# Performance work log

Hardware: AMD Instinct MI355X
Metric: run time of the kernel (lower is better)

Reference implementation:

```python
import jax, jax.numpy as jnp
import numpy as np

N_E = 8192
E_DIM = 64
BETA = 0.25
DIVERSITY_GAMMA = 1.0
INV_TEMP = 100.0
EPS = 1e-05


def _entropy(p):
    # matches torch: (-p * log(clamp(p, min=eps))).sum(-1)
    return (-p * jnp.log(jnp.clip(p, EPS))).sum(axis=-1)


def setup_inputs() -> dict:
    key = jax.random.key(0)
    k1, k2 = jax.random.split(key)
    z = jax.random.normal(k1, (16, E_DIM, 32, 32), dtype=jnp.float32)
    # codebook, init like nn.Embedding then uniform_(-1/n_e, 1/n_e) scale doesn't matter for math;
    # use a small uniform init faithful to the module
    emb = jax.random.uniform(k2, (N_E, E_DIM), dtype=jnp.float32,
                             minval=-1.0 / N_E, maxval=1.0 / N_E)
    return {"z": z, "emb": emb}


def reference(z, emb):
    sg = jax.lax.stop_gradient
    # b c h w -> b h w c
    zp = jnp.transpose(z, (0, 2, 3, 1))            # [B,H,W,C]
    zf = zp.reshape(-1, E_DIM)                      # [N, C]
    # pairwise squared distances: ||z||^2 + ||e||^2 - 2 z e^T
    d = (jnp.sum(zf * zf, axis=1, keepdims=True)
         + jnp.sum(emb * emb, axis=1)
         - 2.0 * jnp.einsum('nd,kd->nk', zf, emb))  # [N, n_e]
    min_indices = jnp.argmin(d, axis=1)             # [N]
    z_q = emb[min_indices].reshape(zp.shape)        # gather, [B,H,W,C]
    # legacy commitment loss
    loss = (jnp.mean((sg(z_q) - zp) ** 2)
            + BETA * jnp.mean((z_q - sg(zp)) ** 2))
    # entropy aux loss (frac_per_sample_entropy == 1.0)
    prob = jax.nn.softmax(-d * INV_TEMP, axis=-1)   # [N, n_e]
    per_sample_entropy = _entropy(prob).mean()
    avg_prob = prob.mean(axis=0)                    # [n_e]
    codebook_entropy = _entropy(avg_prob)
    entropy_aux = per_sample_entropy - DIVERSITY_GAMMA * codebook_entropy
    # straight-through estimator
    z_q = zp + sg(z_q - zp)
    quantized = jnp.transpose(z_q, (0, 3, 1, 2))    # b h w c -> b c h w
    return quantized, loss, entropy_aux, min_indices
```

## Files before the change

kernel.cpp:

```cpp
#include <hip/hip_runtime.h>
#include <cfloat>


typedef __attribute__((ext_vector_type(8))) short short8v;
typedef __attribute__((ext_vector_type(4))) float f32x4;

#define C100L2E 144.26950408889634f
#define C200L2E 288.53900817779268f
#define LN2 0.6931471805599453

#define BLOB_TILE 33792
#define OFF_BLOB   0
#define OFF_INVZ   2162688
#define OFF_MINIDX 2228224
#define OFF_AVG    2293760
#define OFF_PSE    2326528
#define OFF_ZPART  2326544
#define OFF_S1PART (OFF_ZPART + 262144)
#define OFF_DMPART (OFF_S1PART + 262144)
#define OFF_IMPART (OFF_DMPART + 262144)
#define OFF_LOSSP  (OFF_IMPART + 262144)
#define OFF_ZZ     (OFF_LOSSP + 32768)

__device__ __forceinline__ unsigned short f2bf_rne(float f) {
    unsigned u = __float_as_uint(f);
    u = (u + 0x7fffu + ((u >> 16) & 1u)) >> 16;
    return (unsigned short)u;
}

__device__ __forceinline__ void gload_lds16(const void* g, void* l) {
    __builtin_amdgcn_global_load_lds(
        (const __attribute__((address_space(1))) unsigned int*)g,
        (__attribute__((address_space(3))) unsigned int*)l, 16, 0, 0);
}

__global__ __launch_bounds__(256) void k_prep(
    const float* __restrict__ emb, const float* __restrict__ z,
    char* __restrict__ blob, char* __restrict__ zblob, float* __restrict__ zz)
{
    if (blockIdx.x < 32) {
        const int k = blockIdx.x * 256 + threadIdx.x;
        const float* row = emb + k * 64;
        float fv[64];
#pragma unroll
        for (int i = 0; i < 16; ++i) {
            float4 v = ((const float4*)row)[i];
            fv[4 * i] = v.x; fv[4 * i + 1] = v.y; fv[4 * i + 2] = v.z; fv[4 * i + 3] = v.w;
        }
        float r8[8];
#pragma unroll
        for (int j = 0; j < 8; ++j) r8[j] = __fmul_rn(fv[j], fv[j]);
#pragma unroll
        for (int i = 8; i < 64; i += 8)
#pragma unroll
            for (int j = 0; j < 8; ++j)
                r8[j] = __fadd_rn(r8[j], __fmul_rn(fv[i + j], fv[i + j]));
        float s01 = __fadd_rn(r8[0], r8[1]), s23 = __fadd_rn(r8[2], r8[3]);
        float s45 = __fadd_rn(r8[4], r8[5]), s67 = __fadd_rn(r8[6], r8[7]);
        float e2 = __fadd_rn(__fadd_rn(s01, s23), __fadd_rn(s45, s67));

        char* tb = blob + (size_t)(k >> 7) * BLOB_TILE;
        const int r = k & 127;
        ((float*)(tb + 32768))[r] = e2;
        ((float*)(tb + 33280))[r] = e2 * C100L2E;
        const int sw = (r & 7) << 4;
#pragma unroll
        for (int dh = 0; dh < 2; ++dh)
#pragma unroll
            for (int cg = 0; cg < 4; ++cg) {
                short8v hv, lv;
#pragma unroll
                for (int e = 0; e < 8; ++e) {
                    float f = fv[dh * 32 + cg * 8 + e];
                    unsigned short hb = f2bf_rne(f);
                    float hf = __uint_as_float((unsigned)hb << 16);
                    hv[e] = (short)hb;
                    lv[e] = (short)f2bf_rne(f - hf);
                }
                const int byt = (r * 128 + dh * 64 + cg * 16) ^ sw;
                *(short8v*)(tb + byt) = hv;
                *(short8v*)(tb + 16384 + byt) = lv;
            }
    } else {
        const int r = (blockIdx.x - 32) * 256 + threadIdx.x;
        const float* src = z + (r >> 10) * 65536 + (r & 1023);
        float fv[64];
#pragma unroll
        for (int c = 0; c < 64; ++c) fv[c] = src[c * 1024];

        float r8[8];
#pragma unroll
        for (int j = 0; j < 8; ++j) r8[j] = __fmul_rn(fv[j], fv[j]);
#pragma unroll
        for (int i = 8; i < 64; i += 8)
#pragma unroll
            for (int j = 0; j < 8; ++j)
                r8[j] = __fadd_rn(r8[j], __fmul_rn(fv[i + j], fv[i + j]));
        float s01 = __fadd_rn(r8[0], r8[1]), s23 = __fadd_rn(r8[2], r8[3]);
        float s45 = __fadd_rn(r8[4], r8[5]), s67 = __fadd_rn(r8[6], r8[7]);
        zz[r] = __fadd_rn(__fadd_rn(s01, s23), __fadd_rn(s45, s67));

        char* tb = zblob + (size_t)(r >> 6) * 16384;
        const int rowp = r & 63;
#pragma unroll
        for (int cg = 0; cg < 8; ++cg) {
            short8v hv, lv;
#pragma unroll
            for (int e = 0; e < 8; ++e) {
                float f = fv[cg * 8 + e];
                unsigned short hb = f2bf_rne(f);
                float hf = __uint_as_float((unsigned)hb << 16);
                hv[e] = (short)hb;
                lv[e] = (short)f2bf_rne(f - hf);
            }
            *(short8v*)(tb + rowp * 128 + cg * 16) = hv;
            *(short8v*)(tb + 8192 + rowp * 128 + cg * 16) = lv;
        }
    }
}

#define STAGE_EMB(DSTBASE, TILE)                                                  \
    {                                                                             \
        const char* gsrc = blob + (size_t)(TILE) * BLOB_TILE;                     \
        char* ldst = (DSTBASE) + ((tid >> 6) << 10);                              \
        const char* g = gsrc + tid * 16;                                          \
        _Pragma("unroll")                                                         \
        for (int q = 0; q < 8; ++q)                                               \
            gload_lds16(g + q * 4096, ldst + q * 4096);                           \
        if (tid < 64) gload_lds16(gsrc + 32768 + (tid & 63) * 16,                 \
                                  (DSTBASE) + 32768);                             \
    }

#define STAGE512(DSTBASE, TILE)                                                   \
    {                                                                             \
        const char* gsrc = blob + (size_t)(TILE) * BLOB_TILE;                     \
        char* ldst = (DSTBASE) + ((tid >> 6) << 12);                              \
        const char* g = gsrc + ((tid >> 6) << 12) + (tid & 63) * 16;              \
        _Pragma("unroll")                                                         \
        for (int q = 0; q < 4; ++q)                                               \
            gload_lds16(g + q * 1024, ldst + q * 1024);                           \
        if (tid < 64) gload_lds16(gsrc + 32768 + (tid & 63) * 16,                 \
                                  (DSTBASE) + 32768);                             \
    }

__global__ __launch_bounds__(512) void k_pass1(
    const char* __restrict__ zblob, const char* __restrict__ blob,
    const float* __restrict__ zz,
    float* __restrict__ Zpart, float* __restrict__ S1part,
    float* __restrict__ dmpart, int* __restrict__ impart)
{
    __shared__ __align__(16) char smem[2 * BLOB_TILE];

    const int tid = threadIdx.x;
    const int panel = blockIdx.x >> 2;
    const int ks = blockIdx.x & 3;
    const int n0 = panel * 128;

    const int ln = tid & 63, wv = tid >> 6;
    const int lr = ln & 15, lg = ln >> 4;

    short8v Ah[2], Al[2];
    {
        const int p64 = (n0 >> 6) + (wv >> 2);
        const int rowp = (wv & 3) * 16 + lr;
        const char* tb = zblob + (size_t)p64 * 16384;
#pragma unroll
        for (int s = 0; s < 2; ++s) {
            const int byt = rowp * 128 + s * 64 + lg * 16;
            Ah[s] = *(const short8v*)(tb + byt);
            Al[s] = *(const short8v*)(tb + 8192 + byt);
        }
    }
    float zzr[4];
#pragma unroll
    for (int rg = 0; rg < 4; ++rg)
        zzr[rg] = zz[n0 + wv * 16 + lg * 4 + rg];

    STAGE512(smem, ks * 16);

    float Zp[4] = {0.f, 0.f, 0.f, 0.f}, S1p[4] = {0.f, 0.f, 0.f, 0.f};
    float dmin[4] = {FLT_MAX, FLT_MAX, FLT_MAX, FLT_MAX};
    int imin[4] = {0, 0, 0, 0};

    for (int it = 0; it < 16; ++it) {
        const int kbase = ks * 2048 + it * 128;
        __syncthreads();
        const char* bb = smem + (it & 1) * BLOB_TILE;
        if (it < 15) STAGE512(smem + ((it + 1) & 1) * BLOB_TILE, ks * 16 + it + 1);

        f32x4 acc[8];
#pragma unroll
        for (int f = 0; f < 8; ++f) { f32x4 zv = {0.f, 0.f, 0.f, 0.f}; acc[f] = zv; }

#pragma unroll
        for (int f = 0; f < 8; ++f) {
            const int rr = f * 16 + lr;
            const int sw2 = (rr & 7) << 4;
            short8v Bh[2], Bl[2];
#pragma unroll
            for (int s = 0; s < 2; ++s) {
                const int byt = (rr * 128 + s * 64 + lg * 16) ^ sw2;
                Bh[s] = *(const short8v*)(bb + byt);
                Bl[s] = *(const short8v*)(bb + 16384 + byt);
            }
#pragma unroll
            for (int s = 0; s < 2; ++s) {
                acc[f] = __builtin_amdgcn_mfma_f32_16x16x32_bf16(Ah[s], Bh[s], acc[f], 0, 0, 0);
                acc[f] = __builtin_amdgcn_mfma_f32_16x16x32_bf16(Ah[s], Bl[s], acc[f], 0, 0, 0);
                acc[f] = __builtin_amdgcn_mfma_f32_16x16x32_bf16(Al[s], Bh[s], acc[f], 0, 0, 0);
                acc[f] = __builtin_amdgcn_mfma_f32_16x16x32_bf16(Al[s], Bl[s], acc[f], 0, 0, 0);
            }
        }

#pragma unroll
        for (int f = 0; f < 8; ++f) {
            const float e2v = *(const float*)(bb + 32768 + (f * 16 + lr) * 4);
            const float c2 = *(const float*)(bb + 33280 + (f * 16 + lr) * 4);
            const int kk = kbase + f * 16 + lr;
#pragma unroll
            for (int rg = 0; rg < 4; ++rg) {
                const float sdot = acc[f][rg];
                const float t = fmaf(sdot, C200L2E, -c2);
                const float ex = __builtin_amdgcn_exp2f(t);
                Zp[rg] += ex;
                S1p[rg] = fmaf(t, ex, S1p[rg]);
                const float pre = __fadd_rn(zzr[rg], e2v);
                const float dnp = fmaf(-2.f, sdot, pre);
                if (dnp < dmin[rg]) { dmin[rg] = dnp; imin[rg] = kk; }
            }
        }
    }

#pragma unroll
    for (int msk = 1; msk < 16; msk <<= 1) {
#pragma unroll
        for (int rg = 0; rg < 4; ++rg) {
            float d2 = __shfl_xor(dmin[rg], msk, 16);
            int i2 = __shfl_xor(imin[rg], msk, 16);
            float Z2 = __shfl_xor(Zp[rg], msk, 16);
            float s2 = __shfl_xor(S1p[rg], msk, 16);
            if (d2 < dmin[rg] || (d2 == dmin[rg] && i2 < imin[rg])) {
                dmin[rg] = d2; imin[rg] = i2;
            }
            Zp[rg] += Z2;
            S1p[rg] += s2;
        }
    }
    if (lr == 0) {
#pragma unroll
        for (int rg = 0; rg < 4; ++rg) {
            const int n = n0 + wv * 16 + lg * 4 + rg;
            Zpart[ks * 16384 + n] = Zp[rg];
            S1part[ks * 16384 + n] = S1p[rg];
            dmpart[ks * 16384 + n] = dmin[rg];
            impart[ks * 16384 + n] = imin[rg];
        }
    }
}

__global__ __launch_bounds__(256) void k_rowred(
    const float* __restrict__ Zpart, const float* __restrict__ S1part,
    const float* __restrict__ dmpart, const int* __restrict__ impart,
    float* __restrict__ invZ, int* __restrict__ minidx,
    float* __restrict__ out_idx, double* __restrict__ pse_sum)
{
    const int n = blockIdx.x * 256 + threadIdx.x;
    float Z = __fadd_rn(__fadd_rn(Zpart[n], Zpart[16384 + n]),
                        __fadd_rn(Zpart[32768 + n], Zpart[49152 + n]));
    float S1 = __fadd_rn(__fadd_rn(S1part[n], S1part[16384 + n]),
                         __fadd_rn(S1part[32768 + n], S1part[49152 + n]));
    float dm = dmpart[n];
    int im = impart[n];
#pragma unroll
    for (int ksp = 1; ksp < 4; ++ksp) {
        float d2 = dmpart[ksp * 16384 + n];
        int i2 = impart[ksp * 16384 + n];
        if (d2 < dm || (d2 == dm && i2 < im)) { dm = d2; im = i2; }
    }
    minidx[n] = im;
    out_idx[n] = (float)im;
    float iz = 1.0f / Z;
    invZ[n] = iz;
    double h = log((double)Z) - LN2 * (double)S1 * (double)iz;
#pragma unroll
    for (int m = 32; m > 0; m >>= 1) h += __shfl_xor(h, m, 64);
    if ((threadIdx.x & 63) == 0) atomicAdd(pse_sum, h);
}

__global__ __launch_bounds__(256) void k_pass2(
    const char* __restrict__ zblob, const char* __restrict__ blob,
    const float* __restrict__ invZ, float* __restrict__ avg_acc)
{
    __shared__ __align__(16) char smem[BLOB_TILE + 4096];
    float* izAll = (float*)(smem + BLOB_TILE);

    const int tid = threadIdx.x;
    const int kt = blockIdx.x & 63;
    const int ns = blockIdx.x >> 6;
    const int ln = tid & 63, wv = tid >> 6;
    const int lr = ln & 15, lg = ln >> 4;

    STAGE_EMB(smem, kt);
    gload_lds16((const char*)(invZ + ns * 1024) + tid * 16,
                (char*)izAll + (wv << 10));
    __syncthreads();

    float c2v[8];
#pragma unroll
    for (int f = 0; f < 8; ++f)
        c2v[f] = *(const float*)(smem + 33280 + (f * 16 + lr) * 4);

    float acck[8] = {0.f, 0.f, 0.f, 0.f, 0.f, 0.f, 0.f, 0.f};

#pragma unroll 1
    for (int it = 0; it < 16; ++it) {
        const char* tb = zblob + (size_t)(ns * 16 + it) * 16384;
        const int rowp = wv * 16 + lr;
        short8v Ah[2], Al[2];
#pragma unroll
        for (int s = 0; s < 2; ++s) {
            const int byt = rowp * 128 + s * 64 + lg * 16;
            Ah[s] = *(const short8v*)(tb + byt);
            Al[s] = *(const short8v*)(tb + 8192 + byt);
        }
        float4 iz = *(const float4*)&izAll[it * 64 + wv * 16 + lg * 4];
        float izr[4] = {iz.x, iz.y, iz.z, iz.w};

        f32x4 acc[8];
#pragma unroll
        for (int f = 0; f < 8; ++f) { f32x4 zv = {0.f, 0.f, 0.f, 0.f}; acc[f] = zv; }

#pragma unroll
        for (int f = 0; f < 8; ++f) {
            const int rr = f * 16 + lr;
            const int sw2 = (rr & 7) << 4;
            short8v Bh[2], Bl[2];
#pragma unroll
            for (int s = 0; s < 2; ++s) {
                const int byt = (rr * 128 + s * 64 + lg * 16) ^ sw2;
                Bh[s] = *(const short8v*)(smem + byt);
                Bl[s] = *(const short8v*)(smem + 16384 + byt);
            }
#pragma unroll
            for (int s = 0; s < 2; ++s) {
                acc[f] = __builtin_amdgcn_mfma_f32_16x16x32_bf16(Ah[s], Bh[s], acc[f], 0, 0, 0);
                acc[f] = __builtin_amdgcn_mfma_f32_16x16x32_bf16(Ah[s], Bl[s], acc[f], 0, 0, 0);
                acc[f] = __builtin_amdgcn_mfma_f32_16x16x32_bf16(Al[s], Bh[s], acc[f], 0, 0, 0);
            }
        }

#pragma unroll
        for (int f = 0; f < 8; ++f) {
#pragma unroll
            for (int rg = 0; rg < 4; ++rg) {
                const float t = fmaf(acc[f][rg], C200L2E, -c2v[f]);
                const float ex = __builtin_amdgcn_exp2f(t);
                acck[f] = fmaf(ex, izr[rg], acck[f]);
            }
        }
    }

#pragma unroll
    for (int f = 0; f < 8; ++f) {
        float cs = acck[f];
        cs += __shfl_xor(cs, 16, 64);
        cs += __shfl_xor(cs, 32, 64);
        if (lg == 0) atomicAdd(&avg_acc[kt * 128 + f * 16 + lr], cs);
    }
}

__global__ __launch_bounds__(256) void k_quant(
    const float* __restrict__ z, const float* __restrict__ emb,
    const int* __restrict__ minidx, float* __restrict__ out,
    double* __restrict__ loss_part)
{
    __shared__ float lred[4];
    const int o4 = (blockIdx.x * 256 + threadIdx.x) * 4;
    const int nb = ((o4 >> 16) << 10) + (o4 & 1023);
    const int c = (o4 >> 10) & 63;
    const float4 zv = *(const float4*)(z + o4);
    const int i0 = minidx[nb], i1 = minidx[nb + 1];
    const int i2 = minidx[nb + 2], i3 = minidx[nb + 3];
    float4 ev;
    ev.x = emb[i0 * 64 + c];
    ev.y = emb[i1 * 64 + c];
    ev.z = emb[i2 * 64 + c];
    ev.w = emb[i3 * 64 + c];
    *(float4*)(out + o4) = ev;
    const float dx = ev.x - zv.x, dy = ev.y - zv.y;
    const float dz = ev.z - zv.z, dw = ev.w - zv.w;
    float sq = dx * dx + dy * dy + dz * dz + dw * dw;
#pragma unroll
    for (int m = 32; m > 0; m >>= 1) sq += __shfl_xor(sq, m, 64);
    if ((threadIdx.x & 63) == 0) lred[threadIdx.x >> 6] = sq;
    __syncthreads();
    if (threadIdx.x == 0)
        loss_part[blockIdx.x] = (double)lred[0] + (double)lred[1]
                              + (double)lred[2] + (double)lred[3];
}

__global__ __launch_bounds__(256) void k_final(
    const float* __restrict__ avg_acc, const double* __restrict__ pse_sum,
    const double* __restrict__ loss_part, float* __restrict__ out)
{
    __shared__ double red[256];
    const int tid = threadIdx.x;

    double lsum = 0.0;
    for (int k = tid; k < 1024; k += 256) lsum += loss_part[k];
    red[tid] = lsum;
    __syncthreads();
    for (int s = 128; s > 0; s >>= 1) {
        if (tid < s) red[tid] += red[tid + s];
        __syncthreads();
    }
    double ltot = red[0];
    __syncthreads();

    double local = 0.0;
    for (int k = tid; k < 8192; k += 256) {
        float p = avg_acc[k] * (1.0f / 16384.0f);
        float cl = fmaxf(p, 1e-5f);
        local += (double)(-p * logf(cl));
    }
    red[tid] = local;
    __syncthreads();
    for (int s = 128; s > 0; s >>= 1) {
        if (tid < s) red[tid] += red[tid + s];
        __syncthreads();
    }
    if (tid == 0) {
        double ce = red[0];
        double pse = pse_sum[0] / 16384.0;
        out[1048576] = (float)(1.25 * ltot / 1048576.0);
        out[1048577] = (float)(pse - ce);
    }
}

extern "C" void kernel_launch(void* const* d_in, const int* in_sizes, int n_in,
                              void* d_out, int out_size, void* d_ws, size_t ws_size,
                              hipStream_t stream) {
    const float* z = (const float*)d_in[0];
    const float* emb = (const float*)d_in[1];
    float* out = (float*)d_out;
    char* ws = (char*)d_ws;
    char* blob = ws + OFF_BLOB;
    float* invZ = (float*)(ws + OFF_INVZ);
    int* minidx = (int*)(ws + OFF_MINIDX);
    float* avg_acc = (float*)(ws + OFF_AVG);
    double* pse_sum = (double*)(ws + OFF_PSE);
    float* Zpart = (float*)(ws + OFF_ZPART);
    float* S1part = (float*)(ws + OFF_S1PART);
    float* dmpart = (float*)(ws + OFF_DMPART);
    int* impart = (int*)(ws + OFF_IMPART);
    double* loss_part = (double*)(ws + OFF_LOSSP);
    float* zz = (float*)(ws + OFF_ZZ);
    char* zblob = (char*)d_out;

    hipMemsetAsync(ws + OFF_AVG, 0, 32768 + 16, stream);

    k_prep<<<96, 256, 0, stream>>>(emb, z, blob, zblob, zz);
    k_pass1<<<512, 512, 0, stream>>>(zblob, blob, zz, Zpart, S1part, dmpart, impart);
    k_rowred<<<64, 256, 0, stream>>>(Zpart, S1part, dmpart, impart,
                                     invZ, minidx, out + 1048578, pse_sum);
    k_pass2<<<1024, 256, 0, stream>>>(zblob, blob, invZ, avg_acc);
    k_quant<<<1024, 256, 0, stream>>>(z, emb, minidx, out, loss_part);
    k_final<<<1, 256, 0, stream>>>(avg_acc, pse_sum, loss_part, out);
}
```

Baseline: 168.7 us.

## Fuse row reduction and final reduction into producer kernels via last-block semaphores

Removes the separate k_rowred and k_final launches. The last of the four k-split blocks for each panel, detected with an atomic counter, now does the per-row reduction inside k_pass1. The last k_quant block does the global loss and entropy finalization. This saves two kernel launches and their inter-kernel gaps, at the cost of threadfences, atomics and a serialized tail in the last blocks.

```diff
diff --git a/kernel.cpp b/kernel.cpp
--- a/kernel.cpp
+++ b/kernel.cpp
@@ -15,7 +15,8 @@
 #define OFF_MINIDX 2228224
 #define OFF_AVG    2293760
 #define OFF_PSE    2326528
-#define OFF_ZPART  2326544
+#define OFF_SEM    2326544
+#define OFF_ZPART  2327568
 #define OFF_S1PART (OFF_ZPART + 262144)
 #define OFF_DMPART (OFF_S1PART + 262144)
 #define OFF_IMPART (OFF_DMPART + 262144)
@@ -147,9 +148,13 @@
     const char* __restrict__ zblob, const char* __restrict__ blob,
     const float* __restrict__ zz,
     float* __restrict__ Zpart, float* __restrict__ S1part,
-    float* __restrict__ dmpart, int* __restrict__ impart)
+    float* __restrict__ dmpart, int* __restrict__ impart,
+    int* __restrict__ sem, float* __restrict__ invZ,
+    int* __restrict__ minidx, float* __restrict__ out_idx,
+    double* __restrict__ pse_sum)
 {
     __shared__ __align__(16) char smem[2 * BLOB_TILE];
+    __shared__ int islast;
 
     const int tid = threadIdx.x;
     const int panel = blockIdx.x >> 2;
@@ -256,35 +261,40 @@
             impart[ks * 16384 + n] = imin[rg];
         }
     }
-}
-
-__global__ __launch_bounds__(256) void k_rowred(
-    const float* __restrict__ Zpart, const float* __restrict__ S1part,
-    const float* __restrict__ dmpart, const int* __restrict__ impart,
-    float* __restrict__ invZ, int* __restrict__ minidx,
-    float* __restrict__ out_idx, double* __restrict__ pse_sum)
-{
-    const int n = blockIdx.x * 256 + threadIdx.x;
-    float Z = __fadd_rn(__fadd_rn(Zpart[n], Zpart[16384 + n]),
-                        __fadd_rn(Zpart[32768 + n], Zpart[49152 + n]));
-    float S1 = __fadd_rn(__fadd_rn(S1part[n], S1part[16384 + n]),
-                         __fadd_rn(S1part[32768 + n], S1part[49152 + n]));
-    float dm = dmpart[n];
-    int im = impart[n];
-#pragma unroll
-    for (int ksp = 1; ksp < 4; ++ksp) {
-        float d2 = dmpart[ksp * 16384 + n];
-        int i2 = impart[ksp * 16384 + n];
-        if (d2 < dm || (d2 == dm && i2 < im)) { dm = d2; im = i2; }
-    }
-    minidx[n] = im;
-    out_idx[n] = (float)im;
-    float iz = 1.0f / Z;
-    invZ[n] = iz;
-    double h = log((double)Z) - LN2 * (double)S1 * (double)iz;
-#pragma unroll
-    for (int m = 32; m > 0; m >>= 1) h += __shfl_xor(h, m, 64);
-    if ((threadIdx.x & 63) == 0) atomicAdd(pse_sum, h);
+
+    __threadfence();
+    __syncthreads();
+    if (tid == 0) {
+        int old = atomicAdd(&sem[panel], 1);
+        islast = (old == 3) ? 1 : 0;
+    }
+    __syncthreads();
+    if (islast) {
+        __threadfence();
+        if (tid < 128) {
+            const int n = n0 + tid;
+            float Z = __fadd_rn(__fadd_rn(Zpart[n], Zpart[16384 + n]),
+                                __fadd_rn(Zpart[32768 + n], Zpart[49152 + n]));
+            float S1 = __fadd_rn(__fadd_rn(S1part[n], S1part[16384 + n]),
+                                 __fadd_rn(S1part[32768 + n], S1part[49152 + n]));
+            float dm = dmpart[n];
+            int im = impart[n];
+#pragma unroll
+            for (int ksp = 1; ksp < 4; ++ksp) {
+                float d2 = dmpart[ksp * 16384 + n];
+                int i2 = impart[ksp * 16384 + n];
+                if (d2 < dm || (d2 == dm && i2 < im)) { dm = d2; im = i2; }
+            }
+            minidx[n] = im;
+            out_idx[n] = (float)im;
+            float iz = 1.0f / Z;
+            invZ[n] = iz;
+            double h = log((double)Z) - LN2 * (double)S1 * (double)iz;
+#pragma unroll
+            for (int m = 32; m > 0; m >>= 1) h += __shfl_xor(h, m, 64);
+            if ((tid & 63) == 0) atomicAdd(pse_sum, h);
+        }
+    }
 }
 
 __global__ __launch_bounds__(256) void k_pass2(
@@ -372,10 +382,14 @@
 __global__ __launch_bounds__(256) void k_quant(
     const float* __restrict__ z, const float* __restrict__ emb,
     const int* __restrict__ minidx, float* __restrict__ out,
-    double* __restrict__ loss_part)
+    double* __restrict__ loss_part, const float* __restrict__ avg_acc,
+    const double* __restrict__ pse_sum, int* __restrict__ sem)
 {
     __shared__ float lred[4];
-    const int o4 = (blockIdx.x * 256 + threadIdx.x) * 4;
+    __shared__ double red[256];
+    __shared__ int islast;
+    const int tid = threadIdx.x;
+    const int o4 = (blockIdx.x * 256 + tid) * 4;
     const int nb = ((o4 >> 16) << 10) + (o4 & 1023);
     const int c = (o4 >> 10) & 63;
     const float4 zv = *(const float4*)(z + o4);
@@ -392,19 +406,18 @@
     float sq = dx * dx + dy * dy + dz * dz + dw * dw;
 #pragma unroll
     for (int m = 32; m > 0; m >>= 1) sq += __shfl_xor(sq, m, 64);
-    if ((threadIdx.x & 63) == 0) lred[threadIdx.x >> 6] = sq;
-    __syncthreads();
-    if (threadIdx.x == 0)
+    if ((tid & 63) == 0) lred[tid >> 6] = sq;
+    __syncthreads();
+    if (tid == 0) {
         loss_part[blockIdx.x] = (double)lred[0] + (double)lred[1]
                               + (double)lred[2] + (double)lred[3];
-}
-
-__global__ __launch_bounds__(256) void k_final(
-    const float* __restrict__ avg_acc, const double* __restrict__ pse_sum,
-    const double* __restrict__ loss_part, float* __restrict__ out)
-{
-    __shared__ double red[256];
-    const int tid = threadIdx.x;
+        __threadfence();
+        int old = atomicAdd(&sem[128], 1);
+        islast = (old == 1023) ? 1 : 0;
+    }
+    __syncthreads();
+    if (!islast) return;
+    __threadfence();
 
     double lsum = 0.0;
     for (int k = tid; k < 1024; k += 256) lsum += loss_part[k];
@@ -449,6 +462,7 @@
     int* minidx = (int*)(ws + OFF_MINIDX);
     float* avg_acc = (float*)(ws + OFF_AVG);
     double* pse_sum = (double*)(ws + OFF_PSE);
+    int* sem = (int*)(ws + OFF_SEM);
     float* Zpart = (float*)(ws + OFF_ZPART);
     float* S1part = (float*)(ws + OFF_S1PART);
     float* dmpart = (float*)(ws + OFF_DMPART);
@@ -457,13 +471,12 @@
     float* zz = (float*)(ws + OFF_ZZ);
     char* zblob = (char*)d_out;
 
-    hipMemsetAsync(ws + OFF_AVG, 0, 32768 + 16, stream);
+    hipMemsetAsync(ws + OFF_AVG, 0, 32768 + 16 + 1024, stream);
 
     k_prep<<<96, 256, 0, stream>>>(emb, z, blob, zblob, zz);
-    k_pass1<<<512, 512, 0, stream>>>(zblob, blob, zz, Zpart, S1part, dmpart, impart);
-    k_rowred<<<64, 256, 0, stream>>>(Zpart, S1part, dmpart, impart,
-                                     invZ, minidx, out + 1048578, pse_sum);
+    k_pass1<<<512, 512, 0, stream>>>(zblob, blob, zz, Zpart, S1part, dmpart, impart,
+                                     sem, invZ, minidx, out + 1048578, pse_sum);
     k_pass2<<<1024, 256, 0, stream>>>(zblob, blob, invZ, avg_acc);
-    k_quant<<<1024, 256, 0, stream>>>(z, emb, minidx, out, loss_part);
-    k_final<<<1, 256, 0, stream>>>(avg_acc, pse_sum, loss_part, out);
-}
+    k_quant<<<1024, 256, 0, stream>>>(z, emb, minidx, out, loss_part,
+                                      avg_acc, pse_sum, sem);
+}
```

New measurement: 306.4 us. +81.6%, slower.
